# Kernel optimization log

Measured on AMD Instinct MI355X. Metric: run time of the kernel, lower is better.

## Reference

```python
import jax, jax.numpy as jnp
import numpy as np

PDIM = 64
SK = 3
LK = 13

def setup_inputs() -> dict:
    key = jax.random.key(0)
    ks = jax.random.split(key, 6)
    B, C, H, W = 16, 128, 64, 64
    x = jax.random.normal(ks[0], (B, C, H, W), dtype=jnp.float32)
    lk_filter = jax.random.normal(ks[1], (PDIM, PDIM, LK, LK), dtype=jnp.float32) * 0.02
    w1 = jax.random.normal(ks[2], (PDIM // 2, PDIM), dtype=jnp.float32) * 0.1
    b1 = jax.random.normal(ks[3], (PDIM // 2,), dtype=jnp.float32) * 0.1
    w2 = jax.random.normal(ks[4], (PDIM * SK * SK, PDIM // 2), dtype=jnp.float32) * 0.1
    b2 = jax.random.normal(ks[5], (PDIM * SK * SK,), dtype=jnp.float32) * 0.1
    return {"x": x, "lk_filter": lk_filter, "w1": w1, "b1": b1, "w2": w2, "b2": b2}

def reference(x, lk_filter, w1, b1, w2, b2):
    B, C, H, W = x.shape
    x1, x2 = x[:, :PDIM], x[:, PDIM:]

    # dwc_proj: global avg pool -> 1x1 conv -> GELU -> 1x1 conv (per-sample 3x3 kernels)
    pooled = jnp.mean(x[:, :PDIM], axis=(2, 3))                     # [B, pdim]
    h = jax.nn.gelu(pooled @ w1.T + b1, approximate=False)          # [B, pdim//2]
    dyn = (h @ w2.T + b2).reshape(B, PDIM, SK * SK)                 # [B, pdim, 9]

    # dynamic depthwise 3x3 conv, per (batch, channel) kernel, padding=1
    pad = SK // 2
    xp = jnp.pad(x1, ((0, 0), (0, 0), (pad, pad), (pad, pad)))
    patches = jnp.stack([xp[:, :, i:i + H, j:j + W]
                         for i in range(SK) for j in range(SK)], axis=2)  # [B, pdim, 9, H, W]
    x1_dyn = jnp.einsum('bckhw,bck->bchw', patches, dyn)

    # large-kernel dense conv, padding = LK//2 (SAME for odd LK)
    p = LK // 2
    x1_lk = jax.lax.conv_general_dilated(
        x1, lk_filter, window_strides=(1, 1), padding=[(p, p), (p, p)],
        dimension_numbers=('NCHW', 'OIHW', 'NCHW'))

    x1_out = x1_lk + x1_dyn
    return jnp.concatenate([x1_out, x2], axis=1)
```

## Files before the change

### kernel.cpp

```cpp
#include <hip/hip_runtime.h>
#include <hip/hip_bf16.h>

typedef short  short8  __attribute__((ext_vector_type(8)));
typedef float  f32x16  __attribute__((ext_vector_type(16)));

#define XB 16
#define XC 128
#define XH 64
#define XW 64
#define XHW 4096
#define PSTR 72
#define XPROW 76

__device__ __forceinline__ unsigned short f2bf(float f) {
    union { float f; unsigned int u; } v; v.f = f;
    unsigned int r = (v.u + 0x7fffu + ((v.u >> 16) & 1u)) >> 16;
    return (unsigned short)r;
}

__global__ void k_xpad2(const float* __restrict__ x, unsigned short* __restrict__ xpad,
                        float* __restrict__ pooled) {
    int blk = blockIdx.x;
    int b = blk / 76, hp = blk - b * 76;
    int t = threadIdx.x;
    unsigned short* dst = xpad + (size_t)(b * XPROW + hp) * XPROW * PSTR;
    uint4 z = {0u, 0u, 0u, 0u};
    if (hp < 6 || hp >= 70) {
        for (int k = t; k < 684; k += 256) ((uint4*)dst)[k] = z;
        return;
    }
    int h = hp - 6;
    __shared__ float tile[64][65];
    __shared__ float ps[4][64];
    {
        int w = t & 63, cg = t >> 6;
#pragma unroll
        for (int k = 0; k < 16; ++k) {
            int c = cg * 16 + k;
            tile[c][w] = x[(size_t)b * XC * XHW + (size_t)c * XHW + h * 64 + w];
        }
    }
    __syncthreads();
    {
        int c = t & 63, q = t >> 6;
        float s = 0.f;
#pragma unroll
        for (int k = 0; k < 16; ++k) s += tile[c][q * 16 + k];
        ps[q][c] = s;
    }
    __syncthreads();
    if (t < 64) {
        float tot = ps[0][t] + ps[1][t] + ps[2][t] + ps[3][t];
        atomicAdd(pooled + b * 64 + t, tot * (1.f / 4096.f));
    }
    if (t < 108) {
        int px = t / 9, u = t - (t / 9) * 9;
        int ppx = px < 6 ? px : px + 64;
        ((uint4*)(dst + ppx * PSTR))[u] = z;
    }
    {
        int px = t >> 2, cp = t & 3;
        unsigned short tmp[16];
#pragma unroll
        for (int k = 0; k < 16; ++k) tmp[k] = f2bf(tile[cp * 16 + k][px]);
        unsigned int u[8];
#pragma unroll
        for (int k = 0; k < 8; ++k) u[k] = (unsigned int)tmp[2 * k] | ((unsigned int)tmp[2 * k + 1] << 16);
        uint4 v0 = {u[0], u[1], u[2], u[3]};
        uint4 v1 = {u[4], u[5], u[6], u[7]};
        unsigned short* dp = dst + (px + 6) * PSTR + cp * 16;
        *(uint4*)dp = v0;
        *((uint4*)dp + 1) = v1;
        if (cp == 0) ((uint4*)(dst + (px + 6) * PSTR))[8] = z;
    }
}

__global__ void k_mlp(const float* __restrict__ pooled,
                      const float* __restrict__ w1, const float* __restrict__ b1,
                      const float* __restrict__ w2, const float* __restrict__ b2,
                      float* __restrict__ dyn) {
    __shared__ float hbuf[512];
    int t = threadIdx.x;
    if (t < 512) {
        int b = t >> 5, o = t & 31;
        float s = b1[o];
#pragma unroll
        for (int c = 0; c < 64; ++c) s += pooled[b * 64 + c] * w1[o * 64 + c];
        hbuf[b * 32 + o] = 0.5f * s * (1.f + erff(s * 0.70710678118654752f));
    }
    __syncthreads();
    for (int b = 0; b < 16; ++b) {
        float s = b2[t];
#pragma unroll
        for (int i = 0; i < 32; ++i) s += hbuf[b * 32 + i] * w2[t * 32 + i];
        dyn[b * 576 + t] = s;
    }
}

__global__ void k_fpack(const float* __restrict__ lk, unsigned short* __restrict__ fpack) {
    int tidx = blockIdx.x * 256 + threadIdx.x;
    if (tidx >= 169 * 4 * 2 * 64) return;
    int l   = tidx & 63;
    int g   = (tidx >> 6) & 1;
    int ks  = (tidx >> 7) & 3;
    int tap = tidx >> 9;
    int oc  = g * 32 + (l & 31);
    int ic0 = ks * 16 + (l >> 5) * 8;
    unsigned short tmp[8];
#pragma unroll
    for (int e = 0; e < 8; ++e)
        tmp[e] = f2bf(lk[(size_t)(oc * 64 + ic0 + e) * 169 + tap]);
    unsigned int u[4];
#pragma unroll
    for (int k = 0; k < 4; ++k) u[k] = (unsigned int)tmp[2 * k] | ((unsigned int)tmp[2 * k + 1] << 16);
    uint4 v = {u[0], u[1], u[2], u[3]};
    *(uint4*)(fpack + (size_t)tidx * 8) = v;
}

__global__ __launch_bounds__(512, 2) void k_conv(const unsigned short* __restrict__ xpad,
                                                 const unsigned short* __restrict__ fpack,
                                                 const float* __restrict__ dyn,
                                                 const float* __restrict__ x,
                                                 float* __restrict__ out) {
    extern __shared__ unsigned short lds[];
    int blk = blockIdx.x;
    int b = blk >> 4, tile = blk & 15;
    int th = tile >> 2, tw = tile & 3;
    int Y0 = th * 16, X0 = tw * 16;
    int t = threadIdx.x;

    {
        const uint4* xs = (const uint4*)x;
        uint4* od = (uint4*)out;
#pragma unroll
        for (int q = 0; q < 8; ++q) {
            int m4 = blk * 4096 + q * 512 + t;
            int bi = m4 >> 16;
            int rem = m4 & 65535;
            size_t off = (size_t)bi * 131072 + 65536 + rem;
            od[off] = xs[off];
        }
    }

    {
        const unsigned short* srcb = xpad + ((size_t)(b * XPROW + Y0) * XPROW + X0) * PSTR;
        for (int k = t; k < 7056; k += 512) {
            int r = k / 252, o = k - r * 252;
            *(uint4*)(lds + r * 28 * PSTR + o * 8) =
                *(const uint4*)(srcb + (size_t)r * XPROW * PSTR + o * 8);
        }
    }
    __syncthreads();

    int wave = t >> 6, l = t & 63;
    int ks = wave & 3, fc = wave >> 2;
    int l31 = l & 31, lhi = l >> 5;

    int abase = ((l31 >> 3) * 28 + fc * 8 + (l31 & 7)) * PSTR + lhi * 8 + ks * 16;

    f32x16 acc[4][2];
#pragma unroll
    for (int m = 0; m < 4; ++m)
#pragma unroll
        for (int n = 0; n < 2; ++n)
#pragma unroll
            for (int r = 0; r < 16; ++r) acc[m][n][r] = 0.f;

    const unsigned short* fb = fpack + ks * 1024 + l * 8;

#pragma unroll 1
    for (int i = 0; i < 13; ++i) {
        const unsigned short* brow = fb + (size_t)(i * 13) * 4096;
        int arow = abase + i * 28 * PSTR;
#pragma unroll
        for (int j = 0; j < 13; ++j) {
            short8 b0 = *(const short8*)(brow + j * 4096);
            short8 b1 = *(const short8*)(brow + j * 4096 + 512);
            int aoff = arow + j * PSTR;
            __builtin_amdgcn_s_setprio(1);
#pragma unroll
            for (int fr = 0; fr < 4; ++fr) {
                short8 a = *(const short8*)(lds + aoff + fr * 8064);
                acc[fr][0] = __builtin_amdgcn_mfma_f32_32x32x16_bf16(a, b0, acc[fr][0], 0, 0, 0);
                acc[fr][1] = __builtin_amdgcn_mfma_f32_32x32x16_bf16(a, b1, acc[fr][1], 0, 0, 0);
            }
            __builtin_amdgcn_s_setprio(0);
        }
    }

    {
        int ebase = ks * 16 + lhi * 8;
        int e0 = l31 - ebase;
        int e1 = 32 + l31 - ebase;
        const float* dynb = dyn + b * 576;
#pragma unroll
        for (int di = 0; di < 3; ++di)
#pragma unroll
            for (int dj = 0; dj < 3; ++dj) {
                int tp = di * 3 + dj;
                unsigned short v0 = f2bf(dynb[l31 * 9 + tp]);
                unsigned short v1 = f2bf(dynb[(32 + l31) * 9 + tp]);
                short8 b0, b1;
#pragma unroll
                for (int s = 0; s < 8; ++s) {
                    b0[s] = (s == e0) ? (short)v0 : (short)0;
                    b1[s] = (s == e1) ? (short)v1 : (short)0;
                }
                int aoff = abase + ((di + 5) * 28 + (dj + 5)) * PSTR;
#pragma unroll
                for (int fr = 0; fr < 4; ++fr) {
                    short8 a = *(const short8*)(lds + aoff + fr * 8064);
                    acc[fr][0] = __builtin_amdgcn_mfma_f32_32x32x16_bf16(a, b0, acc[fr][0], 0, 0, 0);
                    acc[fr][1] = __builtin_amdgcn_mfma_f32_32x32x16_bf16(a, b1, acc[fr][1], 0, 0, 0);
                }
            }
    }
    __syncthreads();

    float* lf = (float*)lds;
#pragma unroll
    for (int fr = 0; fr < 4; ++fr) {
#pragma unroll
        for (int n = 0; n < 2; ++n)
#pragma unroll
            for (int r = 0; r < 16; ++r) {
                int oc = n * 32 + l31;
                int px = (r >> 2) * 16 + fc * 8 + (r & 3) + 4 * lhi;
                lf[ks * 4160 + oc * 65 + px] = acc[fr][n][r];
            }
        __syncthreads();
#pragma unroll
        for (int k2 = 0; k2 < 8; ++k2) {
            int e = k2 * 512 + t;
            int oc = e >> 6, px = e & 63;
            int idx = oc * 65 + px;
            float s = lf[idx] + lf[4160 + idx] + lf[8320 + idx] + lf[12480 + idx];
            int y = Y0 + fr * 4 + (px >> 4);
            int xx = X0 + (px & 15);
            out[((size_t)(b * XC + oc) * XH + y) * XW + xx] = s;
        }
        __syncthreads();
    }
}

extern "C" void kernel_launch(void* const* d_in, const int* in_sizes, int n_in,
                              void* d_out, int out_size, void* d_ws, size_t ws_size,
                              hipStream_t stream) {
    const float* x  = (const float*)d_in[0];
    const float* lk = (const float*)d_in[1];
    const float* w1 = (const float*)d_in[2];
    const float* b1 = (const float*)d_in[3];
    const float* w2 = (const float*)d_in[4];
    const float* b2 = (const float*)d_in[5];
    float* out = (float*)d_out;

    char* ws = (char*)d_ws;
    float*          pooled = (float*)ws;
    float*          dyn    = (float*)(ws + 4096);
    unsigned short* fpack  = (unsigned short*)(ws + 40960);
    unsigned short* xpad   = (unsigned short*)(ws + 2605056);

    hipMemsetAsync(pooled, 0, 1024 * sizeof(float), stream);
    k_xpad2<<<1216, 256, 0, stream>>>(x, xpad, pooled);
    k_mlp<<<1, 576, 0, stream>>>(pooled, w1, b1, w2, b2, dyn);
    k_fpack<<<338, 256, 0, stream>>>(lk, fpack);
    k_conv<<<256, 512, 112896, stream>>>(xpad, fpack, dyn, x, out);
}
```

Before: 125.8 us.

## Shrink conv tiles to 16x8 with 4-wave blocks and preload filter row

The conv kernel now uses 512 blocks of 256 threads, each covering a 16x8 output tile instead of 16x16. The fc split across waves is dropped, so each wave handles one K-slice over the full tile, and the LDS halo shrinks to 20 columns. All 13 filter fragments for a kernel row are also loaded into registers before the MFMA loop so global loads overlap better. The aim is more blocks to fill the CUs and better latency hiding. In exchange the halo overhead per output rises, filter traffic per output doubles, and the register pressure at 1 block per CU could lower occupancy.

```diff
diff --git a/kernel.cpp b/kernel.cpp
--- a/kernel.cpp
+++ b/kernel.cpp
@@ -117,16 +117,16 @@
     *(uint4*)(fpack + (size_t)tidx * 8) = v;
 }
 
-__global__ __launch_bounds__(512, 2) void k_conv(const unsigned short* __restrict__ xpad,
+__global__ __launch_bounds__(256, 1) void k_conv(const unsigned short* __restrict__ xpad,
                                                  const unsigned short* __restrict__ fpack,
                                                  const float* __restrict__ dyn,
                                                  const float* __restrict__ x,
                                                  float* __restrict__ out) {
     extern __shared__ unsigned short lds[];
     int blk = blockIdx.x;
-    int b = blk >> 4, tile = blk & 15;
-    int th = tile >> 2, tw = tile & 3;
-    int Y0 = th * 16, X0 = tw * 16;
+    int b = blk >> 5, tile = blk & 31;
+    int th = tile >> 3, tw = tile & 7;
+    int Y0 = th * 16, X0 = tw * 8;
     int t = threadIdx.x;
 
     {
@@ -134,7 +134,7 @@
         uint4* od = (uint4*)out;
 #pragma unroll
         for (int q = 0; q < 8; ++q) {
-            int m4 = blk * 4096 + q * 512 + t;
+            int m4 = blk * 2048 + q * 256 + t;
             int bi = m4 >> 16;
             int rem = m4 & 65535;
             size_t off = (size_t)bi * 131072 + 65536 + rem;
@@ -144,19 +144,18 @@
 
     {
         const unsigned short* srcb = xpad + ((size_t)(b * XPROW + Y0) * XPROW + X0) * PSTR;
-        for (int k = t; k < 7056; k += 512) {
-            int r = k / 252, o = k - r * 252;
-            *(uint4*)(lds + r * 28 * PSTR + o * 8) =
+        for (int k = t; k < 5040; k += 256) {
+            int r = k / 180, o = k - r * 180;
+            *(uint4*)(lds + r * 20 * PSTR + o * 8) =
                 *(const uint4*)(srcb + (size_t)r * XPROW * PSTR + o * 8);
         }
     }
     __syncthreads();
 
     int wave = t >> 6, l = t & 63;
-    int ks = wave & 3, fc = wave >> 2;
     int l31 = l & 31, lhi = l >> 5;
 
-    int abase = ((l31 >> 3) * 28 + fc * 8 + (l31 & 7)) * PSTR + lhi * 8 + ks * 16;
+    int abase = ((l31 >> 3) * 20 + (l31 & 7)) * PSTR + lhi * 8 + wave * 16;
 
     f32x16 acc[4][2];
 #pragma unroll
@@ -166,30 +165,34 @@
 #pragma unroll
             for (int r = 0; r < 16; ++r) acc[m][n][r] = 0.f;
 
-    const unsigned short* fb = fpack + ks * 1024 + l * 8;
+    const unsigned short* fb = fpack + wave * 1024 + l * 8;
 
 #pragma unroll 1
     for (int i = 0; i < 13; ++i) {
         const unsigned short* brow = fb + (size_t)(i * 13) * 4096;
-        int arow = abase + i * 28 * PSTR;
+        int arow = abase + i * 20 * PSTR;
+        short8 B0[13], B1[13];
 #pragma unroll
         for (int j = 0; j < 13; ++j) {
-            short8 b0 = *(const short8*)(brow + j * 4096);
-            short8 b1 = *(const short8*)(brow + j * 4096 + 512);
+            B0[j] = *(const short8*)(brow + j * 4096);
+            B1[j] = *(const short8*)(brow + j * 4096 + 512);
+        }
+#pragma unroll
+        for (int j = 0; j < 13; ++j) {
             int aoff = arow + j * PSTR;
             __builtin_amdgcn_s_setprio(1);
 #pragma unroll
             for (int fr = 0; fr < 4; ++fr) {
-                short8 a = *(const short8*)(lds + aoff + fr * 8064);
-                acc[fr][0] = __builtin_amdgcn_mfma_f32_32x32x16_bf16(a, b0, acc[fr][0], 0, 0, 0);
-                acc[fr][1] = __builtin_amdgcn_mfma_f32_32x32x16_bf16(a, b1, acc[fr][1], 0, 0, 0);
+                short8 a = *(const short8*)(lds + aoff + fr * 5760);
+                acc[fr][0] = __builtin_amdgcn_mfma_f32_32x32x16_bf16(a, B0[j], acc[fr][0], 0, 0, 0);
+                acc[fr][1] = __builtin_amdgcn_mfma_f32_32x32x16_bf16(a, B1[j], acc[fr][1], 0, 0, 0);
             }
             __builtin_amdgcn_s_setprio(0);
         }
     }
 
     {
-        int ebase = ks * 16 + lhi * 8;
+        int ebase = wave * 16 + lhi * 8;
         int e0 = l31 - ebase;
         int e1 = 32 + l31 - ebase;
         const float* dynb = dyn + b * 576;
@@ -206,10 +209,10 @@
                     b0[s] = (s == e0) ? (short)v0 : (short)0;
                     b1[s] = (s == e1) ? (short)v1 : (short)0;
                 }
-                int aoff = abase + ((di + 5) * 28 + (dj + 5)) * PSTR;
+                int aoff = abase + ((di + 5) * 20 + (dj + 5)) * PSTR;
 #pragma unroll
                 for (int fr = 0; fr < 4; ++fr) {
-                    short8 a = *(const short8*)(lds + aoff + fr * 8064);
+                    short8 a = *(const short8*)(lds + aoff + fr * 5760);
                     acc[fr][0] = __builtin_amdgcn_mfma_f32_32x32x16_bf16(a, b0, acc[fr][0], 0, 0, 0);
                     acc[fr][1] = __builtin_amdgcn_mfma_f32_32x32x16_bf16(a, b1, acc[fr][1], 0, 0, 0);
                 }
@@ -219,24 +222,23 @@
 
     float* lf = (float*)lds;
 #pragma unroll
-    for (int fr = 0; fr < 4; ++fr) {
+    for (int m = 0; m < 4; ++m) {
 #pragma unroll
         for (int n = 0; n < 2; ++n)
 #pragma unroll
             for (int r = 0; r < 16; ++r) {
                 int oc = n * 32 + l31;
-                int px = (r >> 2) * 16 + fc * 8 + (r & 3) + 4 * lhi;
-                lf[ks * 4160 + oc * 65 + px] = acc[fr][n][r];
+                int p  = (r & 3) + 8 * (r >> 2) + 4 * lhi;
+                lf[wave * 2112 + oc * 33 + p] = acc[m][n][r];
             }
         __syncthreads();
 #pragma unroll
         for (int k2 = 0; k2 < 8; ++k2) {
-            int e = k2 * 512 + t;
-            int oc = e >> 6, px = e & 63;
-            int idx = oc * 65 + px;
-            float s = lf[idx] + lf[4160 + idx] + lf[8320 + idx] + lf[12480 + idx];
-            int y = Y0 + fr * 4 + (px >> 4);
-            int xx = X0 + (px & 15);
+            int e = k2 * 256 + t;
+            int oc = e >> 5, p = e & 31;
+            int idx = oc * 33 + p;
+            float s = lf[idx] + lf[2112 + idx] + lf[4224 + idx] + lf[6336 + idx];
+            int y = Y0 + m * 4 + (p >> 3), xx = X0 + (p & 7);
             out[((size_t)(b * XC + oc) * XH + y) * XW + xx] = s;
         }
         __syncthreads();
@@ -264,5 +266,5 @@
     k_xpad2<<<1216, 256, 0, stream>>>(x, xpad, pooled);
     k_mlp<<<1, 576, 0, stream>>>(pooled, w1, b1, w2, b2, dyn);
     k_fpack<<<338, 256, 0, stream>>>(lk, fpack);
-    k_conv<<<256, 512, 112896, stream>>>(xpad, fpack, dyn, x, out);
-}
+    k_conv<<<512, 256, 80640, stream>>>(xpad, fpack, dyn, x, out);
+}
```

Result: slower. 131.7 us (+4.7%).

## Merge prep kernels and fold dynamic-kernel MLP into the conv kernel

Applied to the files above, without the earlier changes.

The filter-packing kernel is merged into the padding/pooling kernel as extra blocks, and the tiny single-block MLP kernel is removed. Each conv block now recomputes its own sample's GELU hidden layer and 576 dynamic weights into LDS, already converted to bf16. The x2 passthrough copy moves to the end of the conv kernel. This cuts two launches and a serialized single-block kernel, at the cost of redundant MLP work per block and slightly more LDS.

```diff
diff --git a/kernel.cpp b/kernel.cpp
--- a/kernel.cpp
+++ b/kernel.cpp
@@ -18,11 +18,31 @@
     return (unsigned short)r;
 }
 
-__global__ void k_xpad2(const float* __restrict__ x, unsigned short* __restrict__ xpad,
-                        float* __restrict__ pooled) {
+__global__ void k_prep(const float* __restrict__ x, unsigned short* __restrict__ xpad,
+                       float* __restrict__ pooled,
+                       const float* __restrict__ lk, unsigned short* __restrict__ fpack) {
     int blk = blockIdx.x;
+    int t = threadIdx.x;
+    if (blk >= 1216) {
+        int tidx = (blk - 1216) * 256 + t;
+        int l   = tidx & 63;
+        int g   = (tidx >> 6) & 1;
+        int ks  = (tidx >> 7) & 3;
+        int tap = tidx >> 9;
+        int oc  = g * 32 + (l & 31);
+        int ic0 = ks * 16 + (l >> 5) * 8;
+        unsigned short tmp[8];
+#pragma unroll
+        for (int e = 0; e < 8; ++e)
+            tmp[e] = f2bf(lk[(size_t)(oc * 64 + ic0 + e) * 169 + tap]);
+        unsigned int u[4];
+#pragma unroll
+        for (int k = 0; k < 4; ++k) u[k] = (unsigned int)tmp[2 * k] | ((unsigned int)tmp[2 * k + 1] << 16);
+        uint4 v = {u[0], u[1], u[2], u[3]};
+        *(uint4*)(fpack + (size_t)tidx * 8) = v;
+        return;
+    }
     int b = blk / 76, hp = blk - b * 76;
-    int t = threadIdx.x;
     unsigned short* dst = xpad + (size_t)(b * XPROW + hp) * XPROW * PSTR;
     uint4 z = {0u, 0u, 0u, 0u};
     if (hp < 6 || hp >= 70) {
@@ -75,71 +95,29 @@
     }
 }
 
-__global__ void k_mlp(const float* __restrict__ pooled,
-                      const float* __restrict__ w1, const float* __restrict__ b1,
-                      const float* __restrict__ w2, const float* __restrict__ b2,
-                      float* __restrict__ dyn) {
-    __shared__ float hbuf[512];
-    int t = threadIdx.x;
-    if (t < 512) {
-        int b = t >> 5, o = t & 31;
-        float s = b1[o];
-#pragma unroll
-        for (int c = 0; c < 64; ++c) s += pooled[b * 64 + c] * w1[o * 64 + c];
-        hbuf[b * 32 + o] = 0.5f * s * (1.f + erff(s * 0.70710678118654752f));
-    }
-    __syncthreads();
-    for (int b = 0; b < 16; ++b) {
-        float s = b2[t];
-#pragma unroll
-        for (int i = 0; i < 32; ++i) s += hbuf[b * 32 + i] * w2[t * 32 + i];
-        dyn[b * 576 + t] = s;
-    }
-}
-
-__global__ void k_fpack(const float* __restrict__ lk, unsigned short* __restrict__ fpack) {
-    int tidx = blockIdx.x * 256 + threadIdx.x;
-    if (tidx >= 169 * 4 * 2 * 64) return;
-    int l   = tidx & 63;
-    int g   = (tidx >> 6) & 1;
-    int ks  = (tidx >> 7) & 3;
-    int tap = tidx >> 9;
-    int oc  = g * 32 + (l & 31);
-    int ic0 = ks * 16 + (l >> 5) * 8;
-    unsigned short tmp[8];
-#pragma unroll
-    for (int e = 0; e < 8; ++e)
-        tmp[e] = f2bf(lk[(size_t)(oc * 64 + ic0 + e) * 169 + tap]);
-    unsigned int u[4];
-#pragma unroll
-    for (int k = 0; k < 4; ++k) u[k] = (unsigned int)tmp[2 * k] | ((unsigned int)tmp[2 * k + 1] << 16);
-    uint4 v = {u[0], u[1], u[2], u[3]};
-    *(uint4*)(fpack + (size_t)tidx * 8) = v;
-}
-
+#define LDSZ_H 112896
 __global__ __launch_bounds__(512, 2) void k_conv(const unsigned short* __restrict__ xpad,
                                                  const unsigned short* __restrict__ fpack,
-                                                 const float* __restrict__ dyn,
+                                                 const float* __restrict__ pooled,
+                                                 const float* __restrict__ w1, const float* __restrict__ b1,
+                                                 const float* __restrict__ w2, const float* __restrict__ b2,
                                                  const float* __restrict__ x,
                                                  float* __restrict__ out) {
     extern __shared__ unsigned short lds[];
+    unsigned short* ldsDyn = lds + 56448;
+    float* ldsH = (float*)(lds + 57024);
     int blk = blockIdx.x;
     int b = blk >> 4, tile = blk & 15;
     int th = tile >> 2, tw = tile & 3;
     int Y0 = th * 16, X0 = tw * 16;
     int t = threadIdx.x;
 
-    {
-        const uint4* xs = (const uint4*)x;
-        uint4* od = (uint4*)out;
-#pragma unroll
-        for (int q = 0; q < 8; ++q) {
-            int m4 = blk * 4096 + q * 512 + t;
-            int bi = m4 >> 16;
-            int rem = m4 & 65535;
-            size_t off = (size_t)bi * 131072 + 65536 + rem;
-            od[off] = xs[off];
-        }
+    if (t < 32) {
+        float s = b1[t];
+        const float* pb = pooled + b * 64;
+#pragma unroll
+        for (int c = 0; c < 64; ++c) s += pb[c] * w1[t * 64 + c];
+        ldsH[t] = 0.5f * s * (1.f + erff(s * 0.70710678118654752f));
     }
 
     {
@@ -152,6 +130,21 @@
     }
     __syncthreads();
 
+    {
+        float s = b2[t];
+#pragma unroll
+        for (int i = 0; i < 32; ++i) s += ldsH[i] * w2[t * 32 + i];
+        ldsDyn[t] = f2bf(s);
+        if (t < 64) {
+            int o2 = 512 + t;
+            float s2 = b2[o2];
+#pragma unroll
+            for (int i = 0; i < 32; ++i) s2 += ldsH[i] * w2[o2 * 32 + i];
+            ldsDyn[o2] = f2bf(s2);
+        }
+    }
+    __syncthreads();
+
     int wave = t >> 6, l = t & 63;
     int ks = wave & 3, fc = wave >> 2;
     int l31 = l & 31, lhi = l >> 5;
@@ -175,14 +168,14 @@
 #pragma unroll
         for (int j = 0; j < 13; ++j) {
             short8 b0 = *(const short8*)(brow + j * 4096);
-            short8 b1 = *(const short8*)(brow + j * 4096 + 512);
+            short8 b1v = *(const short8*)(brow + j * 4096 + 512);
             int aoff = arow + j * PSTR;
             __builtin_amdgcn_s_setprio(1);
 #pragma unroll
             for (int fr = 0; fr < 4; ++fr) {
                 short8 a = *(const short8*)(lds + aoff + fr * 8064);
                 acc[fr][0] = __builtin_amdgcn_mfma_f32_32x32x16_bf16(a, b0, acc[fr][0], 0, 0, 0);
-                acc[fr][1] = __builtin_amdgcn_mfma_f32_32x32x16_bf16(a, b1, acc[fr][1], 0, 0, 0);
+                acc[fr][1] = __builtin_amdgcn_mfma_f32_32x32x16_bf16(a, b1v, acc[fr][1], 0, 0, 0);
             }
             __builtin_amdgcn_s_setprio(0);
         }
@@ -192,26 +185,25 @@
         int ebase = ks * 16 + lhi * 8;
         int e0 = l31 - ebase;
         int e1 = 32 + l31 - ebase;
-        const float* dynb = dyn + b * 576;
 #pragma unroll
         for (int di = 0; di < 3; ++di)
 #pragma unroll
             for (int dj = 0; dj < 3; ++dj) {
                 int tp = di * 3 + dj;
-                unsigned short v0 = f2bf(dynb[l31 * 9 + tp]);
-                unsigned short v1 = f2bf(dynb[(32 + l31) * 9 + tp]);
-                short8 b0, b1;
+                unsigned short v0 = ldsDyn[l31 * 9 + tp];
+                unsigned short v1 = ldsDyn[(32 + l31) * 9 + tp];
+                short8 b0, b1v;
 #pragma unroll
                 for (int s = 0; s < 8; ++s) {
                     b0[s] = (s == e0) ? (short)v0 : (short)0;
-                    b1[s] = (s == e1) ? (short)v1 : (short)0;
+                    b1v[s] = (s == e1) ? (short)v1 : (short)0;
                 }
                 int aoff = abase + ((di + 5) * 28 + (dj + 5)) * PSTR;
 #pragma unroll
                 for (int fr = 0; fr < 4; ++fr) {
                     short8 a = *(const short8*)(lds + aoff + fr * 8064);
                     acc[fr][0] = __builtin_amdgcn_mfma_f32_32x32x16_bf16(a, b0, acc[fr][0], 0, 0, 0);
-                    acc[fr][1] = __builtin_amdgcn_mfma_f32_32x32x16_bf16(a, b1, acc[fr][1], 0, 0, 0);
+                    acc[fr][1] = __builtin_amdgcn_mfma_f32_32x32x16_bf16(a, b1v, acc[fr][1], 0, 0, 0);
                 }
             }
     }
@@ -240,6 +232,19 @@
             out[((size_t)(b * XC + oc) * XH + y) * XW + xx] = s;
         }
         __syncthreads();
+    }
+
+    {
+        const uint4* xs = (const uint4*)x;
+        uint4* od = (uint4*)out;
+#pragma unroll
+        for (int q = 0; q < 8; ++q) {
+            int m4 = blk * 4096 + q * 512 + t;
+            int bi = m4 >> 16;
+            int rem = m4 & 65535;
+            size_t off = (size_t)bi * 131072 + 65536 + rem;
+            od[off] = xs[off];
+        }
     }
 }
 
@@ -256,13 +261,10 @@
 
     char* ws = (char*)d_ws;
     float*          pooled = (float*)ws;
-    float*          dyn    = (float*)(ws + 4096);
     unsigned short* fpack  = (unsigned short*)(ws + 40960);
     unsigned short* xpad   = (unsigned short*)(ws + 2605056);
 
     hipMemsetAsync(pooled, 0, 1024 * sizeof(float), stream);
-    k_xpad2<<<1216, 256, 0, stream>>>(x, xpad, pooled);
-    k_mlp<<<1, 576, 0, stream>>>(pooled, w1, b1, w2, b2, dyn);
-    k_fpack<<<338, 256, 0, stream>>>(lk, fpack);
-    k_conv<<<256, 512, 112896, stream>>>(xpad, fpack, dyn, x, out);
-}
+    k_prep<<<1554, 256, 0, stream>>>(x, xpad, pooled, lk, fpack);
+    k_conv<<<256, 512, 115328, stream>>>(xpad, fpack, pooled, w1, b1, w2, b2, x, out);
+}
```

Result: faster. 109.0 us (-13.4%).
